# Performance work log

Measured on AMD Instinct MI355X. Metric: run time of the kernel, lower is better.

Reference implementation:

```python
import jax, jax.numpy as jnp
import numpy as np
from jax import lax

B, N = 16, 4096
S1, S2, K = 512, 256, 32
EPS = 1e-5


def setup_inputs() -> dict:
    key = jax.random.key(0)
    ks = jax.random.split(key, 8)
    p = lambda k, shape: jax.random.normal(k, shape, jnp.float32) * 0.05
    return {
        "x": jax.random.normal(ks[0], (B, 3, N), jnp.float32),
        "w1": p(ks[1], (64, 3)),
        "w2": p(ks[2], (64, 64)),
        "g1": jnp.ones(64, jnp.float32), "b1": jnp.zeros(64, jnp.float32),
        "g2": jnp.ones(64, jnp.float32), "b2": jnp.zeros(64, jnp.float32),
        "sg1_w1": p(ks[3], (128, 128)), "sg1_w2": p(ks[4], (128, 128)),
        "sg1_g1": jnp.ones(128, jnp.float32), "sg1_b1": jnp.zeros(128, jnp.float32),
        "sg1_g2": jnp.ones(128, jnp.float32), "sg1_b2": jnp.zeros(128, jnp.float32),
        "sg2_w1": p(ks[5], (256, 256)), "sg2_w2": p(ks[6], (256, 256)),
        "sg2_g1": jnp.ones(256, jnp.float32), "sg2_b1": jnp.zeros(256, jnp.float32),
        "sg2_g2": jnp.ones(256, jnp.float32), "sg2_b2": jnp.zeros(256, jnp.float32),
    }


def fps(coords, s):
    # furthest point sampling, starts at index 0 (as pointnet2 CUDA kernel)
    Bc, Nc, _ = coords.shape
    def step(carry, _):
        dist, far = carry
        centroid = jnp.take_along_axis(coords, far[:, None, None], axis=1)  # [B,1,3]
        d = jnp.sum((coords - centroid) ** 2, -1)                            # [B,N]
        dist = jnp.minimum(dist, d)
        return (dist, jnp.argmax(dist, -1)), far
    init = (jnp.full((Bc, Nc), 1e10, coords.dtype), jnp.zeros((Bc,), jnp.int32))
    _, idxs = lax.scan(step, init, None, length=s)
    return idxs.T  # [B,s]


def gather(pts, idx):
    # pts [B,N,C], idx [B,...] -> [B,...,C]
    return jax.vmap(lambda p, i: p[i])(pts, idx)


def sqdist(a, b):
    # [B,S,3],[B,N,3] -> [B,S,N]
    return (jnp.sum(a ** 2, -1)[..., None] + jnp.sum(b ** 2, -1)[:, None, :]
            - 2.0 * jnp.einsum('bsc,bnc->bsn', a, b))


def bn_relu_grouped(y, g, b):
    # y [B,s,k,O]; BatchNorm1d over (B*s, O, k) => stats over (0,1,2)
    m = y.mean((0, 1, 2), keepdims=True)
    v = y.var((0, 1, 2), keepdims=True)
    return jax.nn.relu((y - m) / jnp.sqrt(v + EPS) * g + b)


def sg_block(f_bnc, coords, s, w1, g1, b1, w2, g2, b2):
    # f_bnc [B,N,C]; coords [B,N,3]
    fidx = fps(coords, s)                      # [B,s]
    new_xyz = gather(coords, fidx)             # [B,s,3]
    new_feat = gather(f_bnc, fidx)             # [B,s,C]
    d = sqdist(new_xyz, coords)                # [B,s,N]
    _, knn_idx = lax.top_k(-d, K)              # [B,s,K]
    grouped = gather(f_bnc, knn_idx)           # [B,s,K,C]
    center = new_feat[:, :, None]              # [B,s,1,C]
    agg = jnp.concatenate([grouped - center,
                           jnp.broadcast_to(center, grouped.shape)], -1)  # [B,s,K,2C]
    y = bn_relu_grouped(jnp.einsum('bskd,od->bsko', agg, w1), g1, b1)
    y = bn_relu_grouped(jnp.einsum('bskd,od->bsko', y, w2), g2, b2)
    return new_xyz, y.max(2)                   # [B,s,O]


def point_cbr(f, w, g, b):
    # f [B,C,N]; conv1d k=1 + BN (stats over (0,2)) + relu
    y = jnp.einsum('bcn,oc->bon', f, w)
    m = y.mean((0, 2), keepdims=True)
    v = y.var((0, 2), keepdims=True)
    return jax.nn.relu((y - m) / jnp.sqrt(v + EPS) * g[None, :, None] + b[None, :, None])


def reference(x, w1, w2, g1, b1, g2, b2,
              sg1_w1, sg1_w2, sg1_g1, sg1_b1, sg1_g2, sg1_b2,
              sg2_w1, sg2_w2, sg2_g1, sg2_b1, sg2_g2, sg2_b2):
    xyz = x.transpose(0, 2, 1)                                  # [B,N,3]
    f = point_cbr(point_cbr(x, w1, g1, b1), w2, g2, b2)         # [B,64,N]
    xyz1, f1 = sg_block(f.transpose(0, 2, 1), xyz, S1,
                        sg1_w1, sg1_g1, sg1_b1, sg1_w2, sg1_g2, sg1_b2)  # f1 [B,S1,128]
    _, f2 = sg_block(f1, xyz1, S2,
                     sg2_w1, sg2_g1, sg2_b1, sg2_w2, sg2_g2, sg2_b2)     # [B,S2,256]
    return f2.transpose(0, 2, 1)                                # [B,256,S2]
```

## Files before the change

kernel.cpp:

```cpp
#include <hip/hip_runtime.h>

#define EPSF 1e-5f
#define NBINS 64
#define STATS_REGION 32768

using short8  = __attribute__((ext_vector_type(8))) short;
using float4v = __attribute__((ext_vector_type(4))) float;

__device__ __forceinline__ unsigned short f2bf(float f){
    unsigned u = __float_as_uint(f);
    unsigned r = u + 0x7FFFu + ((u >> 16) & 1u);
    return (unsigned short)(r >> 16);
}
__device__ __forceinline__ float bf2f(unsigned short h){
    return __uint_as_float(((unsigned)h) << 16);
}
__device__ __forceinline__ unsigned monou(float f){
    unsigned u = __float_as_uint(f);
    return u ^ (((unsigned)((int)u >> 31)) | 0x80000000u);
}

template<int CTRL, int RMASK>
__device__ __forceinline__ float fmax_dpp(float x){
    int xi = __float_as_int(x);
    int yi = __builtin_amdgcn_update_dpp(xi, xi, CTRL, RMASK, 0xf, false);
    return fmaxf(x, __int_as_float(yi));
}
__device__ __forceinline__ float wave_max_dpp(float x){
    x = fmax_dpp<0x111, 0xf>(x);
    x = fmax_dpp<0x112, 0xf>(x);
    x = fmax_dpp<0x114, 0xf>(x);
    x = fmax_dpp<0x118, 0xf>(x);
    x = fmax_dpp<0x142, 0xa>(x);
    x = fmax_dpp<0x143, 0xc>(x);
    return __int_as_float(__builtin_amdgcn_readlane(__float_as_int(x), 63));
}

__device__ __forceinline__ void compute_ss(const float* __restrict__ st,
                                           const float* __restrict__ g,
                                           const float* __restrict__ bb,
                                           float* lss, int C, float invCnt,
                                           int t, int TPB){
    for (int c = t; c < C; c += TPB){
        float s = 0.f, q = 0.f;
        for (int bin = 0; bin < NBINS; bin++){
            s += st[bin * 2 * C + c];
            q += st[bin * 2 * C + C + c];
        }
        float m = s * invCnt;
        float v = q * invCnt - m * m;
        float sc = g[c] / sqrtf(v + EPSF);
        lss[c] = sc;
        lss[C + c] = bb[c] - m * sc;
    }
}


__global__ __launch_bounds__(1024) void stats_x_kernel(const float* __restrict__ x,
                                                       float* __restrict__ xmom){
    int t = threadIdx.x;
    float a[9] = {0,0,0,0,0,0,0,0,0};
    for (int gid = t; gid < 65536; gid += 1024){
        int b = gid >> 12, n = gid & 4095;
        const float* xb = x + (size_t)b * 12288;
        float x0 = xb[n], x1 = xb[4096 + n], x2 = xb[8192 + n];
        a[0] += x0; a[1] += x1; a[2] += x2;
        a[3] += x0*x0; a[4] += x0*x1; a[5] += x0*x2;
        a[6] += x1*x1; a[7] += x1*x2; a[8] += x2*x2;
    }
    __shared__ float red[16][9];
    #pragma unroll
    for (int k = 0; k < 9; k++){
        float v = a[k];
        for (int o = 32; o > 0; o >>= 1) v += __shfl_down(v, o, 64);
        a[k] = v;
    }
    if ((t & 63) == 0){
        #pragma unroll
        for (int k = 0; k < 9; k++) red[t >> 6][k] = a[k];
    }
    __syncthreads();
    if (t == 0){
        #pragma unroll
        for (int k = 0; k < 9; k++){
            float s = 0.f;
            for (int w = 0; w < 16; w++) s += red[w][k];
            xmom[k] = s;
        }
    }
}

__global__ __launch_bounds__(256) void pc_fused_kernel(const float* __restrict__ x,
                                                       const float* __restrict__ w1,
                                                       const float* __restrict__ w2,
                                                       const float* __restrict__ g1,
                                                       const float* __restrict__ b1,
                                                       const float* __restrict__ xmom,
                                                       float* __restrict__ y2t){
    __shared__ float w1s[192];
    __shared__ float wt[4096];
    __shared__ float lss1[128];
    __shared__ float hS[64 * 65];
    int t = threadIdx.x;
    if (t < 192) w1s[t] = w1[t];
    for (int i = t; i < 4096; i += 256){ int o = i & 63, c = i >> 6; wt[c*64+o] = w2[o*64+c]; }
    __syncthreads();
    if (t < 64){
        float mu0 = xmom[0] * (1.f/65536.f), mu1 = xmom[1] * (1.f/65536.f), mu2 = xmom[2] * (1.f/65536.f);
        float M00 = xmom[3] * (1.f/65536.f), M01 = xmom[4] * (1.f/65536.f), M02 = xmom[5] * (1.f/65536.f);
        float M11 = xmom[6] * (1.f/65536.f), M12 = xmom[7] * (1.f/65536.f), M22 = xmom[8] * (1.f/65536.f);
        float a = w1s[t*3], b = w1s[t*3+1], c = w1s[t*3+2];
        float mo = a*mu0 + b*mu1 + c*mu2;
        float e2 = a*a*M00 + b*b*M11 + c*c*M22 + 2.f*(a*b*M01 + a*c*M02 + b*c*M12);
        float var = e2 - mo*mo;
        float sc = g1[t] / sqrtf(var + EPSF);
        lss1[t] = sc;
        lss1[64 + t] = b1[t] - mo * sc;
    }
    __syncthreads();
    int p = t & 63, cg = t >> 6;
    int point = blockIdx.x * 64 + p;
    int b = point >> 12, n = point & 4095;
    const float* xb = x + (size_t)b * 12288;
    float x0 = xb[n], x1 = xb[4096 + n], x2 = xb[8192 + n];
    #pragma unroll
    for (int i = 0; i < 16; i++){
        int c = cg * 16 + i;
        float y1 = x0 * w1s[c*3] + x1 * w1s[c*3+1] + x2 * w1s[c*3+2];
        hS[p * 65 + c] = fmaxf(y1 * lss1[c] + lss1[64 + c], 0.f);
    }
    __syncthreads();
    float4v acc[4];
    #pragma unroll
    for (int i = 0; i < 4; i++) acc[i] = (float4v){0.f,0.f,0.f,0.f};
    for (int c = 0; c < 64; c++){
        float hv = hS[p * 65 + c];
        #pragma unroll
        for (int i = 0; i < 4; i++){
            float4v w4 = *(const float4v*)&wt[c*64 + cg*16 + i*4];
            acc[i] += hv * w4;
        }
    }
    float* dst = y2t + (size_t)point * 64 + cg * 16;
    #pragma unroll
    for (int i = 0; i < 4; i++) *(float4v*)(dst + i*4) = acc[i];
}

__global__ __launch_bounds__(256) void stats_y2_kernel(const float* __restrict__ y2t,
                                                       float* __restrict__ sums){
    int t = threadIdx.x, blk = blockIdx.x;
    int o = t & 63, rg = t >> 6;
    float s = 0.f, q = 0.f;
    for (int j = 0; j < 64; j++){
        int row = blk * 256 + j * 4 + rg;
        float v = y2t[(size_t)row * 64 + o];
        s += v; q += v * v;
    }
    __shared__ float rs[4][64], rq[4][64];
    rs[rg][o] = s; rq[rg][o] = q;
    __syncthreads();
    if (t < 64){
        float ss = rs[0][t] + rs[1][t] + rs[2][t] + rs[3][t];
        float qq = rq[0][t] + rq[1][t] + rq[2][t] + rq[3][t];
        float* dst = sums + (size_t)(blk & (NBINS - 1)) * 128;
        atomicAdd(&dst[t], ss);
        atomicAdd(&dst[64 + t], qq);
    }
}

template<int NP, int SO, int TPB, bool STRIDED>
__global__ __launch_bounds__(TPB) void fps_kernel(const float* __restrict__ coords,
                                                  int* __restrict__ fidx,
                                                  float* __restrict__ xyz_out){
    __shared__ float lx[NP], ly[NP], lz[NP];
    constexpr int W = TPB / 64;
    __shared__ unsigned long long red[2][W];
    const int b = blockIdx.x, t = threadIdx.x;
    constexpr int P = NP / TPB;
    const float* cb = coords + (size_t)b * 3 * NP;
    float px[P], py[P], pz[P], dist[P];
    #pragma unroll
    for (int i = 0; i < P; i++){
        int n = i * TPB + t;
        float X, Y, Z;
        if (STRIDED){ X = cb[n]; Y = cb[NP + n]; Z = cb[2*NP + n]; }
        else        { X = cb[n*3]; Y = cb[n*3+1]; Z = cb[n*3+2]; }
        lx[n] = X; ly[n] = Y; lz[n] = Z;
    }
    __syncthreads();
    #pragma unroll
    for (int i = 0; i < P; i++){
        int n = t * P + i;
        px[i] = lx[n]; py[i] = ly[n]; pz[i] = lz[n];
        dist[i] = 1e10f;
    }
    int cur = 0;
    for (int it = 0; it < SO; ++it){
        if (t == 0){
            fidx[b * SO + it] = cur;
            float* xo = xyz_out + ((size_t)b * SO + it) * 3;
            xo[0] = lx[cur]; xo[1] = ly[cur]; xo[2] = lz[cur];
        }
        float cx = lx[cur], cy = ly[cur], cz = lz[cur];
        float bd = -1.f;
        int bn = 0;
        {
            #pragma clang fp contract(off)
            #pragma unroll
            for (int i = 0; i < P; i++){
                float dx = px[i] - cx, dy = py[i] - cy, dz = pz[i] - cz;
                float d = (dx*dx + dy*dy) + dz*dz;
                float nd = fminf(dist[i], d);
                dist[i] = nd;
                if (nd > bd){ bd = nd; bn = t * P + i; }
            }
        }
        float wm = wave_max_dpp(bd);
        unsigned long long msk = __ballot(bd == wm);
        int wl = (int)(__ffsll(msk) - 1);
        int n_w = __builtin_amdgcn_readlane(bn, wl);
        if constexpr (W == 1){
            cur = n_w;
        } else {
            int par = it & 1;
            if ((t & 63) == 0){
                red[par][t >> 6] = ((unsigned long long)__float_as_uint(wm) << 32)
                                 | (unsigned)(0xFFFFFFFFu - (unsigned)n_w);
            }
            __syncthreads();
            unsigned long long best = red[par][0];
            #pragma unroll
            for (int j = 1; j < W; j++){
                unsigned long long v = red[par][j];
                best = best > v ? best : v;
            }
            cur = (int)(0xFFFFFFFFu - (unsigned)(best & 0xFFFFFFFFull));
        }
    }
}


template<int NC, int SO, bool STRIDED>
__global__ __launch_bounds__(64) void knn_kernel(const float* __restrict__ coords,
                                                 const float* __restrict__ samp,
                                                 int* __restrict__ knno){
    const int blk = blockIdx.x;
    const int b = blk / SO, s = blk % SO;
    const int lane = threadIdx.x;
    const float* cb = coords + (size_t)b * 3 * NC;
    const float* a = samp + ((size_t)b * SO + s) * 3;
    float ax = a[0], ay = a[1], az = a[2];
    float asq = ax*ax + ay*ay + az*az;
    constexpr int J = NC / 64;
    unsigned long long t8[8];
    #pragma unroll
    for (int i = 0; i < 8; i++) t8[i] = ~0ULL;
    for (int j = 0; j < J; j++){
        int n = j * 64 + lane;
        float bx, by, bz;
        if (STRIDED){ bx = cb[n]; by = cb[NC + n]; bz = cb[2*NC + n]; }
        else        { bx = cb[n*3]; by = cb[n*3+1]; bz = cb[n*3+2]; }
        float bsq = bx*bx + by*by + bz*bz;
        float dot = ax*bx + ay*by + az*bz;
        float d = (asq + bsq) - 2.0f * dot;
        unsigned long long key = ((unsigned long long)monou(d) << 32) | (unsigned)n;
        if (key < t8[7]){
            t8[7] = key;
            #pragma unroll
            for (int i = 6; i >= 0; i--){
                if (t8[i] > t8[i+1]){ unsigned long long tm = t8[i]; t8[i] = t8[i+1]; t8[i+1] = tm; }
            }
        }
    }
    unsigned long long cur = t8[0];
    int myout = 0;
    bool bad = false;
    int popped = 0;
    for (int r = 0; r < 32; r++){
        unsigned long long m = cur;
        #pragma unroll
        for (int o2 = 32; o2 > 0; o2 >>= 1){
            unsigned long long v = __shfl_xor(m, o2, 64);
            m = m < v ? m : v;
        }
        if (lane == r) myout = (int)(unsigned)(m & 0xFFFFFFFFull);
        if (cur == m){
            #pragma unroll
            for (int i = 0; i < 7; i++) t8[i] = t8[i+1];
            t8[7] = ~0ULL;
            cur = t8[0];
            popped++;
            if (J > 8 && popped == 8 && r < 31) bad = true;
        }
    }
    if (__any(bad)){
        unsigned long long last = 0;
        for (int r = 0; r < 32; r++){
            unsigned long long mk = ~0ULL;
            for (int j = 0; j < J; j++){
                int n = j * 64 + lane;
                float bx, by, bz;
                if (STRIDED){ bx = cb[n]; by = cb[NC + n]; bz = cb[2*NC + n]; }
                else        { bx = cb[n*3]; by = cb[n*3+1]; bz = cb[n*3+2]; }
                float bsq = bx*bx + by*by + bz*bz;
                float dot = ax*bx + ay*by + az*bz;
                float d = (asq + bsq) - 2.0f * dot;
                unsigned long long key = ((unsigned long long)monou(d) << 32) | (unsigned)n;
                if (key > last && key < mk) mk = key;
            }
            unsigned long long m = mk;
            #pragma unroll
            for (int o2 = 32; o2 > 0; o2 >>= 1){
                unsigned long long v = __shfl_xor(m, o2, 64);
                m = m < v ? m : v;
            }
            if (lane == r) myout = (int)(unsigned)(m & 0xFFFFFFFFull);
            last = m;
        }
    }
    if (lane < 32) knno[((size_t)b * SO + s) * 32 + lane] = myout;
}


template<int O, int D>
__device__ __forceinline__ void pack_body(const float* __restrict__ w,
                                          unsigned short* __restrict__ pk, int tid){
    constexpr int CH = D / 32;
    constexpr int TOT = (O/16) * CH * 64;
    if (tid >= TOT) return;
    int lane = tid & 63;
    int fc = tid >> 6;
    int ch = fc % CH;
    int ot = fc / CH;
    int o  = ot * 16 + (lane & 15);
    int kb = ch * 32 + (lane >> 4) * 8;
    #pragma unroll
    for (int j = 0; j < 8; j++) pk[(size_t)tid * 8 + j] = f2bf(w[(size_t)o * D + kb + j]);
}

__global__ __launch_bounds__(256) void pack_all_kernel(const float* w1, const float* w2,
                                                       const float* w3, const float* w4,
                                                       unsigned short* p1, unsigned short* p2,
                                                       unsigned short* p3, unsigned short* p4){
    int blk = blockIdx.x, t = threadIdx.x;
    if (blk < 8)       pack_body<128,128>(w1, p1, blk * 256 + t);
    else if (blk < 16) pack_body<128,128>(w2, p2, (blk - 8) * 256 + t);
    else if (blk < 48) pack_body<256,256>(w3, p3, (blk - 16) * 256 + t);
    else               pack_body<256,256>(w4, p4, (blk - 48) * 256 + t);
}

template<int D, int O>
__device__ __forceinline__ void mfma_store_y(const short* A, const short* wp,
                                             unsigned short* Y, float* lsum, float* lsq,
                                             int blk, int t){
    constexpr int RS = D + 8;
    constexpr int CH = D / 32;
    constexpr int OT = O / 16;
    constexpr int OPW = OT / 4;
    int lane = t & 63, wv = t >> 6;
    int col = lane & 15, quad = lane >> 4;
    for (int oi = 0; oi < OPW; ++oi){
        int ot = wv * OPW + oi;
        for (int mt = 0; mt < 4; ++mt){
            float4v acc = {0.f, 0.f, 0.f, 0.f};
            #pragma unroll
            for (int ch = 0; ch < CH; ++ch){
                short8 a  = *(const short8*)(A + (mt*16 + col) * RS + ch*32 + quad*8);
                short8 bf = *(const short8*)(wp + ((size_t)(ot*CH + ch) * 64 + lane) * 8);
                acc = __builtin_amdgcn_mfma_f32_16x16x32_bf16(a, bf, acc, 0, 0, 0);
            }
            float s4 = 0.f, q4 = 0.f;
            size_t rowbase = (size_t)blk * 64 + mt * 16 + quad * 4;
            #pragma unroll
            for (int r = 0; r < 4; r++){
                float v = acc[r];
                s4 += v; q4 += v * v;
                Y[(rowbase + r) * O + ot * 16 + col] = f2bf(v);
            }
            s4 += __shfl_xor(s4, 16, 64); s4 += __shfl_xor(s4, 32, 64);
            q4 += __shfl_xor(q4, 16, 64); q4 += __shfl_xor(q4, 32, 64);
            if (quad == 0){ lsum[ot*16 + col] += s4; lsq[ot*16 + col] += q4; }
        }
    }
}

template<int D, int O>
__device__ __forceinline__ void mfma_maxmin(const short* A, const short* wp,
                                            float2* mxmn, float* lsum, float* lsq,
                                            int blk, int t){
    constexpr int RS = D + 8;
    constexpr int CH = D / 32;
    constexpr int OT = O / 16;
    constexpr int OPW = OT / 4;
    int lane = t & 63, wv = t >> 6;
    int col = lane & 15, quad = lane >> 4;
    for (int oi = 0; oi < OPW; ++oi){
        int ot = wv * OPW + oi;
        float mx[2] = {-1e30f, -1e30f}, mn[2] = {1e30f, 1e30f};
        for (int mt = 0; mt < 4; ++mt){
            float4v acc = {0.f, 0.f, 0.f, 0.f};
            #pragma unroll
            for (int ch = 0; ch < CH; ++ch){
                short8 a  = *(const short8*)(A + (mt*16 + col) * RS + ch*32 + quad*8);
                short8 bf = *(const short8*)(wp + ((size_t)(ot*CH + ch) * 64 + lane) * 8);
                acc = __builtin_amdgcn_mfma_f32_16x16x32_bf16(a, bf, acc, 0, 0, 0);
            }
            int g = mt >> 1;
            float s4 = 0.f, q4 = 0.f;
            #pragma unroll
            for (int r = 0; r < 4; r++){
                float v = acc[r];
                s4 += v; q4 += v * v;
                mx[g] = fmaxf(mx[g], v);
                mn[g] = fminf(mn[g], v);
            }
            s4 += __shfl_xor(s4, 16, 64); s4 += __shfl_xor(s4, 32, 64);
            q4 += __shfl_xor(q4, 16, 64); q4 += __shfl_xor(q4, 32, 64);
            if (quad == 0){ lsum[ot*16 + col] += s4; lsq[ot*16 + col] += q4; }
        }
        #pragma unroll
        for (int g = 0; g < 2; g++){
            mx[g] = fmaxf(mx[g], __shfl_xor(mx[g], 16, 64));
            mx[g] = fmaxf(mx[g], __shfl_xor(mx[g], 32, 64));
            mn[g] = fminf(mn[g], __shfl_xor(mn[g], 16, 64));
            mn[g] = fminf(mn[g], __shfl_xor(mn[g], 32, 64));
            if (quad == 0){
                mxmn[((size_t)(blk * 2 + g)) * O + ot * 16 + col] = make_float2(mx[g], mn[g]);
            }
        }
    }
}

template<int DH, int O, int S, int NPTS, int MODE>
__global__ __launch_bounds__(256) void gemm1_kernel(const void* __restrict__ fsrc,
                                                    const float* __restrict__ fst,
                                                    const float* __restrict__ fg,
                                                    const float* __restrict__ fb,
                                                    float finv,
                                                    const int* __restrict__ fidx,
                                                    const int* __restrict__ knn,
                                                    const short* __restrict__ wp,
                                                    unsigned short* __restrict__ Y,
                                                    float* __restrict__ sums){
    constexpr int D = 2 * DH;
    constexpr int RS = D + 8;
    __shared__ __align__(16) short A[64 * RS];
    __shared__ float lsum[O], lsq[O];
    __shared__ float lssf[2 * DH];
    int t = threadIdx.x;
    for (int i = t; i < O; i += 256){ lsum[i] = 0.f; lsq[i] = 0.f; }
    compute_ss(fst, fg, fb, lssf, DH, finv, t, 256);
    __syncthreads();
    int blk = blockIdx.x;
    for (int g = 0; g < 2; ++g){
        int gid = blk * 2 + g;
        int b = gid / S;
        int cidx = fidx[gid];
        int kk = t >> 3;
        int p  = t & 7;
        int nb = knn[(size_t)gid * 32 + kk];
        constexpr int E = D / 8;
        int d0 = p * E;
        short* row = A + (g * 32 + kk) * RS;
        if (MODE == 1){
            const float* fcp = (const float*)fsrc + ((size_t)b * NPTS + cidx) * DH;
            const float* fnp = (const float*)fsrc + ((size_t)b * NPTS + nb) * DH;
            #pragma unroll
            for (int e = 0; e < E; e++){
                int d = d0 + e;
                float v;
                if (d < DH){
                    float a = fmaxf(fnp[d] * lssf[d] + lssf[DH + d], 0.f);
                    float c = fmaxf(fcp[d] * lssf[d] + lssf[DH + d], 0.f);
                    v = a - c;
                } else {
                    v = fmaxf(fcp[d - DH] * lssf[d - DH] + lssf[DH + d - DH], 0.f);
                }
                row[d] = (short)f2bf(v);
            }
        } else {
            const float2* fcp = (const float2*)fsrc + ((size_t)b * NPTS + cidx) * DH;
            const float2* fnp = (const float2*)fsrc + ((size_t)b * NPTS + nb) * DH;
            #pragma unroll
            for (int e = 0; e < E; e++){
                int d = d0 + e;
                float v;
                if (d < DH){
                    float sc = lssf[d], sh = lssf[DH + d];
                    float2 a2 = fnp[d], c2 = fcp[d];
                    float av = fmaxf((sc > 0.f ? a2.x : a2.y) * sc + sh, 0.f);
                    float cv = fmaxf((sc > 0.f ? c2.x : c2.y) * sc + sh, 0.f);
                    v = av - cv;
                } else {
                    int dd = d - DH;
                    float sc = lssf[dd], sh = lssf[DH + dd];
                    float2 c2 = fcp[dd];
                    v = fmaxf((sc > 0.f ? c2.x : c2.y) * sc + sh, 0.f);
                }
                row[d] = (short)f2bf(v);
            }
        }
    }
    __syncthreads();
    mfma_store_y<D, O>(A, wp, Y, lsum, lsq, blk, t);
    __syncthreads();
    float* dst = sums + (size_t)(blk & (NBINS - 1)) * 2 * O;
    for (int i = t; i < O; i += 256){
        atomicAdd(&dst[i], lsum[i]);
        atomicAdd(&dst[O + i], lsq[i]);
    }
}

template<int D, int O>
__global__ __launch_bounds__(256) void gemm2m_kernel(const unsigned short* __restrict__ Yin,
                                                     const float* __restrict__ st,
                                                     const float* __restrict__ g,
                                                     const float* __restrict__ bb,
                                                     float inv,
                                                     const short* __restrict__ wp,
                                                     float2* __restrict__ mxmn,
                                                     float* __restrict__ sums){
    constexpr int RS = D + 8;
    __shared__ __align__(16) short A[64 * RS];
    __shared__ float lsum[O], lsq[O];
    __shared__ float lss[2 * D];
    int t = threadIdx.x;
    for (int i = t; i < O; i += 256){ lsum[i] = 0.f; lsq[i] = 0.f; }
    compute_ss(st, g, bb, lss, D, inv, t, 256);
    __syncthreads();
    int blk = blockIdx.x;
    {
        int row = t >> 2;
        int d0 = (t & 3) * (D / 4);
        const unsigned short* src = Yin + ((size_t)blk * 64 + row) * D + d0;
        short* dst = A + row * RS + d0;
        #pragma unroll
        for (int e = 0; e < D/4; e++){
            float v = bf2f(src[e]);
            int d = d0 + e;
            v = fmaxf(v * lss[d] + lss[D + d], 0.f);
            dst[e] = (short)f2bf(v);
        }
    }
    __syncthreads();
    mfma_maxmin<D, O>(A, wp, mxmn, lsum, lsq, blk, t);
    __syncthreads();
    float* dst = sums + (size_t)(blk & (NBINS - 1)) * 2 * O;
    for (int i = t; i < O; i += 256){
        atomicAdd(&dst[i], lsum[i]);
        atomicAdd(&dst[O + i], lsq[i]);
    }
}

__global__ __launch_bounds__(256) void final_out_kernel(const float2* __restrict__ mxmn,
                                                        const float* __restrict__ st,
                                                        const float* __restrict__ g,
                                                        const float* __restrict__ bb,
                                                        float inv,
                                                        float* __restrict__ out){
    __shared__ float lss[512];
    __shared__ float tile[64][65];
    int t = threadIdx.x;
    compute_ss(st, g, bb, lss, 256, inv, t, 256);
    __syncthreads();
    int blk = blockIdx.x;
    int b = blk >> 4;
    int ot = (blk >> 2) & 3, stt = blk & 3;
    int o_in = t & 63, sg = t >> 6;
    int o = ot * 64 + o_in;
    float sc = lss[o], sh = lss[256 + o];
    for (int si = 0; si < 16; si++){
        int s = stt * 64 + sg * 16 + si;
        int row = b * 256 + s;
        float2 v2 = mxmn[(size_t)row * 256 + o];
        float v = (sc > 0.f ? v2.x : v2.y) * sc + sh;
        tile[sg * 16 + si][o_in] = fmaxf(v, 0.f);
    }
    __syncthreads();
    int s_in = t & 63, og = t >> 6;
    for (int oj = 0; oj < 16; oj++){
        int oo = ot * 64 + og * 16 + oj;
        out[(size_t)b * 65536 + (size_t)oo * 256 + stt * 64 + s_in] = tile[s_in][og * 16 + oj];
    }
}

extern "C" void kernel_launch(void* const* d_in, const int* in_sizes, int n_in,
                              void* d_out, int out_size, void* d_ws, size_t ws_size,
                              hipStream_t stream) {
    const float* x    = (const float*)d_in[0];
    const float* w1   = (const float*)d_in[1];
    const float* w2   = (const float*)d_in[2];
    const float* g1   = (const float*)d_in[3];
    const float* b1   = (const float*)d_in[4];
    const float* g2   = (const float*)d_in[5];
    const float* b2   = (const float*)d_in[6];
    const float* s1w1 = (const float*)d_in[7];
    const float* s1w2 = (const float*)d_in[8];
    const float* s1g1 = (const float*)d_in[9];
    const float* s1b1 = (const float*)d_in[10];
    const float* s1g2 = (const float*)d_in[11];
    const float* s1b2 = (const float*)d_in[12];
    const float* s2w1 = (const float*)d_in[13];
    const float* s2w2 = (const float*)d_in[14];
    const float* s2g1 = (const float*)d_in[15];
    const float* s2b1 = (const float*)d_in[16];
    const float* s2g2 = (const float*)d_in[17];
    const float* s2b2 = (const float*)d_in[18];
    float* out = (float*)d_out;

    char* ws = (char*)d_ws;
    size_t off = 0;
    auto take = [&](size_t bytes){ size_t r = off; off += (bytes + 255) & ~(size_t)255; return r; };
    float* y2t     = (float*)(ws + take(16u*4096u*64u*4u));
    float2* mxmn1  = (float2*)(ws + take(8192u*128u*8u));
    float2* mxmn2  = (float2*)(ws + take(4096u*256u*8u));
    int*   fidx1   = (int*)  (ws + take(16u*512u*4u));
    float* xyz1    = (float*)(ws + take(16u*512u*3u*4u));
    int*   fidx2   = (int*)  (ws + take(16u*256u*4u));
    float* xyz2    = (float*)(ws + take(16u*256u*3u*4u));
    int*   knn1    = (int*)  (ws + take(16u*512u*32u*4u));
    int*   knn2    = (int*)  (ws + take(16u*256u*32u*4u));
    unsigned short* wp1 = (unsigned short*)(ws + take(128u*128u*2u));
    unsigned short* wp2 = (unsigned short*)(ws + take(128u*128u*2u));
    unsigned short* wp3 = (unsigned short*)(ws + take(256u*256u*2u));
    unsigned short* wp4 = (unsigned short*)(ws + take(256u*256u*2u));
    float* stats   = (float*)(ws + take(6u*STATS_REGION*4u));
    char*  regA    = ws + take(67108864u);
    (void)in_sizes; (void)n_in; (void)out_size; (void)ws_size;

    float* xmom    = stats + 0*STATS_REGION;
    float* stY2    = stats + 1*STATS_REGION;
    float* stG1a   = stats + 2*STATS_REGION;
    float* stG2a   = stats + 3*STATS_REGION;
    float* stG1b   = stats + 4*STATS_REGION;
    float* stG2b   = stats + 5*STATS_REGION;

    hipMemsetAsync(stats, 0, 6u*STATS_REGION*4u, stream);

    pack_all_kernel<<<80, 256, 0, stream>>>(s1w1, s1w2, s2w1, s2w2, wp1, wp2, wp3, wp4);

    stats_x_kernel<<<1, 1024, 0, stream>>>(x, xmom);
    pc_fused_kernel<<<1024, 256, 0, stream>>>(x, w1, w2, g1, b1, xmom, y2t);
    stats_y2_kernel<<<256, 256, 0, stream>>>(y2t, stY2);

    fps_kernel<4096,512,256,true><<<16, 256, 0, stream>>>(x, fidx1, xyz1);
    knn_kernel<4096,512,true><<<8192, 64, 0, stream>>>(x, xyz1, knn1);

    unsigned short* Y1 = (unsigned short*)regA;
    gemm1_kernel<64,128,512,4096,1><<<4096, 256, 0, stream>>>(
        y2t, stY2, g2, b2, 1.f/65536.f, fidx1, knn1, (const short*)wp1, Y1, stG1a);
    gemm2m_kernel<128,128><<<4096, 256, 0, stream>>>(
        Y1, stG1a, s1g1, s1b1, 1.f/262144.f, (const short*)wp2, mxmn1, stG2a);

    fps_kernel<512,256,64,false><<<16, 64, 0, stream>>>(xyz1, fidx2, xyz2);
    knn_kernel<512,256,false><<<4096, 64, 0, stream>>>(xyz1, xyz2, knn2);

    gemm1_kernel<128,256,256,512,2><<<2048, 256, 0, stream>>>(
        mxmn1, stG2a, s1g2, s1b2, 1.f/262144.f, fidx2, knn2, (const short*)wp3, Y1, stG1b);
    gemm2m_kernel<256,256><<<2048, 256, 0, stream>>>(
        Y1, stG1b, s2g1, s2b1, 1.f/131072.f, (const short*)wp4, mxmn2, stG2b);
    final_out_kernel<<<256, 256, 0, stream>>>(
        mxmn2, stG2b, s2g2, s2b2, 1.f/131072.f, out);
}
```

Measured before the change: 1.029 ms.

## Merge independent stages into combined kernels to overlap FPS with GEMM work

Independent pipeline stages are packed into shared launches by splitting on block index. Examples are FPS1 with the pointwise conv, stats_y2 with knn1, FPS2 with the first grouped GEMM, and knn2 with the second GEMM. Kernel bodies become device functions using dynamic shared memory. The intent is to hide the long serial FPS loops under parallel work and cut launch count. A risk is that heterogeneous blocks share resource limits (shared memory sized for the larger body), which may reduce occupancy of the GEMM parts.

```diff
diff --git a/kernel.cpp b/kernel.cpp
--- a/kernel.cpp
+++ b/kernel.cpp
@@ -55,139 +55,29 @@
     }
 }
 
-
-__global__ __launch_bounds__(1024) void stats_x_kernel(const float* __restrict__ x,
-                                                       float* __restrict__ xmom){
-    int t = threadIdx.x;
-    float a[9] = {0,0,0,0,0,0,0,0,0};
-    for (int gid = t; gid < 65536; gid += 1024){
-        int b = gid >> 12, n = gid & 4095;
-        const float* xb = x + (size_t)b * 12288;
-        float x0 = xb[n], x1 = xb[4096 + n], x2 = xb[8192 + n];
-        a[0] += x0; a[1] += x1; a[2] += x2;
-        a[3] += x0*x0; a[4] += x0*x1; a[5] += x0*x2;
-        a[6] += x1*x1; a[7] += x1*x2; a[8] += x2*x2;
-    }
-    __shared__ float red[16][9];
+template<int NP, int SO, int AW, bool STRIDED>
+__device__ void fps_body(char* smem, const float* __restrict__ coords,
+                         int* __restrict__ fidx, float* __restrict__ xyz_out, int b){
+    float* lx = (float*)smem;
+    float* ly = lx + NP;
+    float* lz = ly + NP;
+    unsigned long long* red = (unsigned long long*)(lz + NP);
+    const int t = threadIdx.x;
+    const float* cb = coords + (size_t)b * 3 * NP;
+    constexpr int PS = NP / 256;
     #pragma unroll
-    for (int k = 0; k < 9; k++){
-        float v = a[k];
-        for (int o = 32; o > 0; o >>= 1) v += __shfl_down(v, o, 64);
-        a[k] = v;
-    }
-    if ((t & 63) == 0){
-        #pragma unroll
-        for (int k = 0; k < 9; k++) red[t >> 6][k] = a[k];
-    }
-    __syncthreads();
-    if (t == 0){
-        #pragma unroll
-        for (int k = 0; k < 9; k++){
-            float s = 0.f;
-            for (int w = 0; w < 16; w++) s += red[w][k];
-            xmom[k] = s;
-        }
-    }
-}
-
-__global__ __launch_bounds__(256) void pc_fused_kernel(const float* __restrict__ x,
-                                                       const float* __restrict__ w1,
-                                                       const float* __restrict__ w2,
-                                                       const float* __restrict__ g1,
-                                                       const float* __restrict__ b1,
-                                                       const float* __restrict__ xmom,
-                                                       float* __restrict__ y2t){
-    __shared__ float w1s[192];
-    __shared__ float wt[4096];
-    __shared__ float lss1[128];
-    __shared__ float hS[64 * 65];
-    int t = threadIdx.x;
-    if (t < 192) w1s[t] = w1[t];
-    for (int i = t; i < 4096; i += 256){ int o = i & 63, c = i >> 6; wt[c*64+o] = w2[o*64+c]; }
-    __syncthreads();
-    if (t < 64){
-        float mu0 = xmom[0] * (1.f/65536.f), mu1 = xmom[1] * (1.f/65536.f), mu2 = xmom[2] * (1.f/65536.f);
-        float M00 = xmom[3] * (1.f/65536.f), M01 = xmom[4] * (1.f/65536.f), M02 = xmom[5] * (1.f/65536.f);
-        float M11 = xmom[6] * (1.f/65536.f), M12 = xmom[7] * (1.f/65536.f), M22 = xmom[8] * (1.f/65536.f);
-        float a = w1s[t*3], b = w1s[t*3+1], c = w1s[t*3+2];
-        float mo = a*mu0 + b*mu1 + c*mu2;
-        float e2 = a*a*M00 + b*b*M11 + c*c*M22 + 2.f*(a*b*M01 + a*c*M02 + b*c*M12);
-        float var = e2 - mo*mo;
-        float sc = g1[t] / sqrtf(var + EPSF);
-        lss1[t] = sc;
-        lss1[64 + t] = b1[t] - mo * sc;
-    }
-    __syncthreads();
-    int p = t & 63, cg = t >> 6;
-    int point = blockIdx.x * 64 + p;
-    int b = point >> 12, n = point & 4095;
-    const float* xb = x + (size_t)b * 12288;
-    float x0 = xb[n], x1 = xb[4096 + n], x2 = xb[8192 + n];
-    #pragma unroll
-    for (int i = 0; i < 16; i++){
-        int c = cg * 16 + i;
-        float y1 = x0 * w1s[c*3] + x1 * w1s[c*3+1] + x2 * w1s[c*3+2];
-        hS[p * 65 + c] = fmaxf(y1 * lss1[c] + lss1[64 + c], 0.f);
-    }
-    __syncthreads();
-    float4v acc[4];
-    #pragma unroll
-    for (int i = 0; i < 4; i++) acc[i] = (float4v){0.f,0.f,0.f,0.f};
-    for (int c = 0; c < 64; c++){
-        float hv = hS[p * 65 + c];
-        #pragma unroll
-        for (int i = 0; i < 4; i++){
-            float4v w4 = *(const float4v*)&wt[c*64 + cg*16 + i*4];
-            acc[i] += hv * w4;
-        }
-    }
-    float* dst = y2t + (size_t)point * 64 + cg * 16;
-    #pragma unroll
-    for (int i = 0; i < 4; i++) *(float4v*)(dst + i*4) = acc[i];
-}
-
-__global__ __launch_bounds__(256) void stats_y2_kernel(const float* __restrict__ y2t,
-                                                       float* __restrict__ sums){
-    int t = threadIdx.x, blk = blockIdx.x;
-    int o = t & 63, rg = t >> 6;
-    float s = 0.f, q = 0.f;
-    for (int j = 0; j < 64; j++){
-        int row = blk * 256 + j * 4 + rg;
-        float v = y2t[(size_t)row * 64 + o];
-        s += v; q += v * v;
-    }
-    __shared__ float rs[4][64], rq[4][64];
-    rs[rg][o] = s; rq[rg][o] = q;
-    __syncthreads();
-    if (t < 64){
-        float ss = rs[0][t] + rs[1][t] + rs[2][t] + rs[3][t];
-        float qq = rq[0][t] + rq[1][t] + rq[2][t] + rq[3][t];
-        float* dst = sums + (size_t)(blk & (NBINS - 1)) * 128;
-        atomicAdd(&dst[t], ss);
-        atomicAdd(&dst[64 + t], qq);
-    }
-}
-
-template<int NP, int SO, int TPB, bool STRIDED>
-__global__ __launch_bounds__(TPB) void fps_kernel(const float* __restrict__ coords,
-                                                  int* __restrict__ fidx,
-                                                  float* __restrict__ xyz_out){
-    __shared__ float lx[NP], ly[NP], lz[NP];
-    constexpr int W = TPB / 64;
-    __shared__ unsigned long long red[2][W];
-    const int b = blockIdx.x, t = threadIdx.x;
-    constexpr int P = NP / TPB;
-    const float* cb = coords + (size_t)b * 3 * NP;
-    float px[P], py[P], pz[P], dist[P];
-    #pragma unroll
-    for (int i = 0; i < P; i++){
-        int n = i * TPB + t;
+    for (int i = 0; i < PS; i++){
+        int n = i * 256 + t;
         float X, Y, Z;
         if (STRIDED){ X = cb[n]; Y = cb[NP + n]; Z = cb[2*NP + n]; }
         else        { X = cb[n*3]; Y = cb[n*3+1]; Z = cb[n*3+2]; }
         lx[n] = X; ly[n] = Y; lz[n] = Z;
     }
     __syncthreads();
+    if (AW == 1 && t >= 64) return;
+    constexpr int TPB = AW * 64;
+    constexpr int P = NP / TPB;
+    float px[P], py[P], pz[P], dist[P];
     #pragma unroll
     for (int i = 0; i < P; i++){
         int n = t * P + i;
@@ -219,19 +109,19 @@
         unsigned long long msk = __ballot(bd == wm);
         int wl = (int)(__ffsll(msk) - 1);
         int n_w = __builtin_amdgcn_readlane(bn, wl);
-        if constexpr (W == 1){
+        if constexpr (AW == 1){
             cur = n_w;
         } else {
             int par = it & 1;
             if ((t & 63) == 0){
-                red[par][t >> 6] = ((unsigned long long)__float_as_uint(wm) << 32)
-                                 | (unsigned)(0xFFFFFFFFu - (unsigned)n_w);
+                red[par * AW + (t >> 6)] = ((unsigned long long)__float_as_uint(wm) << 32)
+                                         | (unsigned)(0xFFFFFFFFu - (unsigned)n_w);
             }
             __syncthreads();
-            unsigned long long best = red[par][0];
-            #pragma unroll
-            for (int j = 1; j < W; j++){
-                unsigned long long v = red[par][j];
+            unsigned long long best = red[par * AW];
+            #pragma unroll
+            for (int j = 1; j < AW; j++){
+                unsigned long long v = red[par * AW + j];
                 best = best > v ? best : v;
             }
             cur = (int)(0xFFFFFFFFu - (unsigned)(best & 0xFFFFFFFFull));
@@ -239,14 +129,12 @@
     }
 }
 
-
 template<int NC, int SO, bool STRIDED>
-__global__ __launch_bounds__(64) void knn_kernel(const float* __restrict__ coords,
-                                                 const float* __restrict__ samp,
-                                                 int* __restrict__ knno){
-    const int blk = blockIdx.x;
-    const int b = blk / SO, s = blk % SO;
-    const int lane = threadIdx.x;
+__device__ void knn_body(const float* __restrict__ coords,
+                         const float* __restrict__ samp,
+                         int* __restrict__ knno, int row){
+    const int b = row / SO, s = row % SO;
+    const int lane = threadIdx.x & 63;
     const float* cb = coords + (size_t)b * 3 * NC;
     const float* a = samp + ((size_t)b * SO + s) * 3;
     float ax = a[0], ay = a[1], az = a[2];
@@ -321,6 +209,59 @@
     if (lane < 32) knno[((size_t)b * SO + s) * 32 + lane] = myout;
 }
 
+__device__ void pc_body(char* smem, const float* __restrict__ x,
+                        const float* __restrict__ w1, const float* __restrict__ w2,
+                        const float* __restrict__ g1, const float* __restrict__ b1,
+                        const float* __restrict__ xmom, float* __restrict__ y2t, int blk){
+    float* w1s  = (float*)smem;
+    float* wt   = w1s + 192;
+    float* lss1 = wt + 4096;
+    float* hS   = lss1 + 128;
+    int t = threadIdx.x;
+    if (t < 192) w1s[t] = w1[t];
+    for (int i = t; i < 4096; i += 256){ int o = i & 63, c = i >> 6; wt[c*64+o] = w2[o*64+c]; }
+    __syncthreads();
+    if (t < 64){
+        float mu0 = xmom[0] * (1.f/65536.f), mu1 = xmom[1] * (1.f/65536.f), mu2 = xmom[2] * (1.f/65536.f);
+        float M00 = xmom[3] * (1.f/65536.f), M01 = xmom[4] * (1.f/65536.f), M02 = xmom[5] * (1.f/65536.f);
+        float M11 = xmom[6] * (1.f/65536.f), M12 = xmom[7] * (1.f/65536.f), M22 = xmom[8] * (1.f/65536.f);
+        float a = w1s[t*3], b = w1s[t*3+1], c = w1s[t*3+2];
+        float mo = a*mu0 + b*mu1 + c*mu2;
+        float e2 = a*a*M00 + b*b*M11 + c*c*M22 + 2.f*(a*b*M01 + a*c*M02 + b*c*M12);
+        float var = e2 - mo*mo;
+        float sc = g1[t] / sqrtf(var + EPSF);
+        lss1[t] = sc;
+        lss1[64 + t] = b1[t] - mo * sc;
+    }
+    __syncthreads();
+    int p = t & 63, cg = t >> 6;
+    int point = blk * 64 + p;
+    int b = point >> 12, n = point & 4095;
+    const float* xb = x + (size_t)b * 12288;
+    float x0 = xb[n], x1 = xb[4096 + n], x2 = xb[8192 + n];
+    #pragma unroll
+    for (int i = 0; i < 16; i++){
+        int c = cg * 16 + i;
+        float y1 = x0 * w1s[c*3] + x1 * w1s[c*3+1] + x2 * w1s[c*3+2];
+        hS[p * 65 + c] = fmaxf(y1 * lss1[c] + lss1[64 + c], 0.f);
+    }
+    __syncthreads();
+    float4v acc[4];
+    #pragma unroll
+    for (int i = 0; i < 4; i++) acc[i] = (float4v){0.f,0.f,0.f,0.f};
+    for (int c = 0; c < 64; c++){
+        float hv = hS[p * 65 + c];
+        #pragma unroll
+        for (int i = 0; i < 4; i++){
+            float4v w4 = *(const float4v*)&wt[c*64 + cg*16 + i*4];
+            acc[i] += hv * w4;
+        }
+    }
+    float* dst = y2t + (size_t)point * 64 + cg * 16;
+    #pragma unroll
+    for (int i = 0; i < 4; i++) *(float4v*)(dst + i*4) = acc[i];
+}
+
 
 template<int O, int D>
 __device__ __forceinline__ void pack_body(const float* __restrict__ w,
@@ -338,25 +279,13 @@
     for (int j = 0; j < 8; j++) pk[(size_t)tid * 8 + j] = f2bf(w[(size_t)o * D + kb + j]);
 }
 
-__global__ __launch_bounds__(256) void pack_all_kernel(const float* w1, const float* w2,
-                                                       const float* w3, const float* w4,
-                                                       unsigned short* p1, unsigned short* p2,
-                                                       unsigned short* p3, unsigned short* p4){
-    int blk = blockIdx.x, t = threadIdx.x;
-    if (blk < 8)       pack_body<128,128>(w1, p1, blk * 256 + t);
-    else if (blk < 16) pack_body<128,128>(w2, p2, (blk - 8) * 256 + t);
-    else if (blk < 48) pack_body<256,256>(w3, p3, (blk - 16) * 256 + t);
-    else               pack_body<256,256>(w4, p4, (blk - 48) * 256 + t);
-}
-
 template<int D, int O>
 __device__ __forceinline__ void mfma_store_y(const short* A, const short* wp,
                                              unsigned short* Y, float* lsum, float* lsq,
                                              int blk, int t){
     constexpr int RS = D + 8;
     constexpr int CH = D / 32;
-    constexpr int OT = O / 16;
-    constexpr int OPW = OT / 4;
+    constexpr int OPW = (O / 16) / 4;
     int lane = t & 63, wv = t >> 6;
     int col = lane & 15, quad = lane >> 4;
     for (int oi = 0; oi < OPW; ++oi){
@@ -390,8 +319,7 @@
                                             int blk, int t){
     constexpr int RS = D + 8;
     constexpr int CH = D / 32;
-    constexpr int OT = O / 16;
-    constexpr int OPW = OT / 4;
+    constexpr int OPW = (O / 16) / 4;
     int lane = t & 63, wv = t >> 6;
     int col = lane & 15, quad = lane >> 4;
     for (int oi = 0; oi < OPW; ++oi){
@@ -432,26 +360,22 @@
 }
 
 template<int DH, int O, int S, int NPTS, int MODE>
-__global__ __launch_bounds__(256) void gemm1_kernel(const void* __restrict__ fsrc,
-                                                    const float* __restrict__ fst,
-                                                    const float* __restrict__ fg,
-                                                    const float* __restrict__ fb,
-                                                    float finv,
-                                                    const int* __restrict__ fidx,
-                                                    const int* __restrict__ knn,
-                                                    const short* __restrict__ wp,
-                                                    unsigned short* __restrict__ Y,
-                                                    float* __restrict__ sums){
+__device__ void gemm1_body(char* smem, const void* __restrict__ fsrc,
+                           const float* __restrict__ fst, const float* __restrict__ fg,
+                           const float* __restrict__ fb, float finv,
+                           const int* __restrict__ fidx, const int* __restrict__ knn,
+                           const short* __restrict__ wp, unsigned short* __restrict__ Y,
+                           float* __restrict__ sums, int blk){
     constexpr int D = 2 * DH;
     constexpr int RS = D + 8;
-    __shared__ __align__(16) short A[64 * RS];
-    __shared__ float lsum[O], lsq[O];
-    __shared__ float lssf[2 * DH];
+    short* A    = (short*)smem;
+    float* lsum = (float*)(smem + 64*RS*2);
+    float* lsq  = lsum + O;
+    float* lssf = lsq + O;
     int t = threadIdx.x;
     for (int i = t; i < O; i += 256){ lsum[i] = 0.f; lsq[i] = 0.f; }
     compute_ss(fst, fg, fb, lssf, DH, finv, t, 256);
     __syncthreads();
-    int blk = blockIdx.x;
     for (int g = 0; g < 2; ++g){
         int gid = blk * 2 + g;
         int b = gid / S;
@@ -512,23 +436,20 @@
 }
 
 template<int D, int O>
-__global__ __launch_bounds__(256) void gemm2m_kernel(const unsigned short* __restrict__ Yin,
-                                                     const float* __restrict__ st,
-                                                     const float* __restrict__ g,
-                                                     const float* __restrict__ bb,
-                                                     float inv,
-                                                     const short* __restrict__ wp,
-                                                     float2* __restrict__ mxmn,
-                                                     float* __restrict__ sums){
+__device__ void gemm2m_body(char* smem, const unsigned short* __restrict__ Yin,
+                            const float* __restrict__ st, const float* __restrict__ g,
+                            const float* __restrict__ bb, float inv,
+                            const short* __restrict__ wp, float2* __restrict__ mxmn,
+                            float* __restrict__ sums, int blk){
     constexpr int RS = D + 8;
-    __shared__ __align__(16) short A[64 * RS];
-    __shared__ float lsum[O], lsq[O];
-    __shared__ float lss[2 * D];
+    short* A    = (short*)smem;
+    float* lsum = (float*)(smem + 64*RS*2);
+    float* lsq  = lsum + O;
+    float* lss  = lsq + O;
     int t = threadIdx.x;
     for (int i = t; i < O; i += 256){ lsum[i] = 0.f; lsq[i] = 0.f; }
     compute_ss(st, g, bb, lss, D, inv, t, 256);
     __syncthreads();
-    int blk = blockIdx.x;
     {
         int row = t >> 2;
         int d0 = (t & 3) * (D / 4);
@@ -550,6 +471,147 @@
         atomicAdd(&dst[i], lsum[i]);
         atomicAdd(&dst[O + i], lsq[i]);
     }
+}
+
+
+__global__ __launch_bounds__(256) void k1_statsx_pack(const float* __restrict__ x,
+                                                      float* __restrict__ xmom,
+                                                      const float* w1, const float* w2,
+                                                      const float* w3, const float* w4,
+                                                      unsigned short* p1, unsigned short* p2,
+                                                      unsigned short* p3, unsigned short* p4){
+    int blk = blockIdx.x, t = threadIdx.x;
+    if (blk == 0){
+        float a[9] = {0,0,0,0,0,0,0,0,0};
+        for (int gid = t; gid < 65536; gid += 256){
+            int b = gid >> 12, n = gid & 4095;
+            const float* xb = x + (size_t)b * 12288;
+            float x0 = xb[n], x1 = xb[4096 + n], x2 = xb[8192 + n];
+            a[0] += x0; a[1] += x1; a[2] += x2;
+            a[3] += x0*x0; a[4] += x0*x1; a[5] += x0*x2;
+            a[6] += x1*x1; a[7] += x1*x2; a[8] += x2*x2;
+        }
+        __shared__ float red[4][9];
+        #pragma unroll
+        for (int k = 0; k < 9; k++){
+            float v = a[k];
+            for (int o = 32; o > 0; o >>= 1) v += __shfl_down(v, o, 64);
+            a[k] = v;
+        }
+        if ((t & 63) == 0){
+            #pragma unroll
+            for (int k = 0; k < 9; k++) red[t >> 6][k] = a[k];
+        }
+        __syncthreads();
+        if (t == 0){
+            #pragma unroll
+            for (int k = 0; k < 9; k++)
+                xmom[k] = red[0][k] + red[1][k] + red[2][k] + red[3][k];
+        }
+    } else {
+        int pb = blk - 1;
+        if (pb < 8)       pack_body<128,128>(w1, p1, pb * 256 + t);
+        else if (pb < 16) pack_body<128,128>(w2, p2, (pb - 8) * 256 + t);
+        else if (pb < 48) pack_body<256,256>(w3, p3, (pb - 16) * 256 + t);
+        else              pack_body<256,256>(w4, p4, (pb - 48) * 256 + t);
+    }
+}
+
+__global__ __launch_bounds__(256) void k2_fps1_pc(const float* __restrict__ x,
+                                                  int* __restrict__ fidx1, float* __restrict__ xyz1,
+                                                  const float* w1, const float* w2,
+                                                  const float* g1, const float* b1,
+                                                  const float* __restrict__ xmom,
+                                                  float* __restrict__ y2t){
+    extern __shared__ char smem[];
+    if (blockIdx.x < 16) fps_body<4096,512,4,true>(smem, x, fidx1, xyz1, blockIdx.x);
+    else                 pc_body(smem, x, w1, w2, g1, b1, xmom, y2t, blockIdx.x - 16);
+}
+
+__global__ __launch_bounds__(256) void k3_statsy2_knn1(const float* __restrict__ y2t,
+                                                       float* __restrict__ stY2,
+                                                       const float* __restrict__ x,
+                                                       const float* __restrict__ xyz1,
+                                                       int* __restrict__ knn1){
+    int t = threadIdx.x;
+    if (blockIdx.x < 256){
+        int blk = blockIdx.x;
+        int o = t & 63, rg = t >> 6;
+        float s = 0.f, q = 0.f;
+        for (int j = 0; j < 64; j++){
+            int row = blk * 256 + j * 4 + rg;
+            float v = y2t[(size_t)row * 64 + o];
+            s += v; q += v * v;
+        }
+        __shared__ float rs[4][64], rq[4][64];
+        rs[rg][o] = s; rq[rg][o] = q;
+        __syncthreads();
+        if (t < 64){
+            float ss = rs[0][t] + rs[1][t] + rs[2][t] + rs[3][t];
+            float qq = rq[0][t] + rq[1][t] + rq[2][t] + rq[3][t];
+            float* dst = stY2 + (size_t)(blk & (NBINS - 1)) * 128;
+            atomicAdd(&dst[t], ss);
+            atomicAdd(&dst[64 + t], qq);
+        }
+    } else {
+        int row = (blockIdx.x - 256) * 4 + (t >> 6);
+        knn_body<4096,512,true>(x, xyz1, knn1, row);
+    }
+}
+
+__global__ __launch_bounds__(256) void k4_fps2_gemm1a(const float* __restrict__ xyz1,
+                                                      int* __restrict__ fidx2, float* __restrict__ xyz2,
+                                                      const float* __restrict__ y2t,
+                                                      const float* __restrict__ stY2,
+                                                      const float* g2, const float* b2,
+                                                      const int* __restrict__ fidx1,
+                                                      const int* __restrict__ knn1,
+                                                      const short* __restrict__ wp1,
+                                                      unsigned short* __restrict__ Y1,
+                                                      float* __restrict__ stG1a){
+    extern __shared__ char smem[];
+    if (blockIdx.x < 16)
+        fps_body<512,256,1,false>(smem, xyz1, fidx2, xyz2, blockIdx.x);
+    else
+        gemm1_body<64,128,512,4096,1>(smem, y2t, stY2, g2, b2, 1.f/65536.f,
+                                      fidx1, knn1, wp1, Y1, stG1a, blockIdx.x - 16);
+}
+
+__global__ __launch_bounds__(256) void k5_knn2_gemm2ma(const float* __restrict__ xyz1,
+                                                       const float* __restrict__ xyz2,
+                                                       int* __restrict__ knn2,
+                                                       const unsigned short* __restrict__ Y1,
+                                                       const float* __restrict__ stG1a,
+                                                       const float* s1g1, const float* s1b1,
+                                                       const short* __restrict__ wp2,
+                                                       float2* __restrict__ mxmn1,
+                                                       float* __restrict__ stG2a){
+    extern __shared__ char smem[];
+    if (blockIdx.x < 1024){
+        int row = blockIdx.x * 4 + (threadIdx.x >> 6);
+        knn_body<512,256,false>(xyz1, xyz2, knn2, row);
+    } else {
+        gemm2m_body<128,128>(smem, Y1, stG1a, s1g1, s1b1, 1.f/262144.f,
+                             wp2, mxmn1, stG2a, blockIdx.x - 1024);
+    }
+}
+
+template<int DH, int O, int S, int NPTS, int MODE>
+__global__ __launch_bounds__(256) void gemm1_kernel(const void* fsrc, const float* fst,
+                                                    const float* fg, const float* fb, float finv,
+                                                    const int* fidx, const int* knn,
+                                                    const short* wp, unsigned short* Y,
+                                                    float* sums){
+    extern __shared__ char smem[];
+    gemm1_body<DH,O,S,NPTS,MODE>(smem, fsrc, fst, fg, fb, finv, fidx, knn, wp, Y, sums, blockIdx.x);
+}
+
+template<int D, int O>
+__global__ __launch_bounds__(256) void gemm2m_kernel(const unsigned short* Yin, const float* st,
+                                                     const float* g, const float* bb, float inv,
+                                                     const short* wp, float2* mxmn, float* sums){
+    extern __shared__ char smem[];
+    gemm2m_body<D,O>(smem, Yin, st, g, bb, inv, wp, mxmn, sums, blockIdx.x);
 }
 
 __global__ __launch_bounds__(256) void final_out_kernel(const float2* __restrict__ mxmn,
@@ -635,30 +697,20 @@
     float* stG1b   = stats + 4*STATS_REGION;
     float* stG2b   = stats + 5*STATS_REGION;
 
+    unsigned short* Y1 = (unsigned short*)regA;
+
     hipMemsetAsync(stats, 0, 6u*STATS_REGION*4u, stream);
 
-    pack_all_kernel<<<80, 256, 0, stream>>>(s1w1, s1w2, s2w1, s2w2, wp1, wp2, wp3, wp4);
-
-    stats_x_kernel<<<1, 1024, 0, stream>>>(x, xmom);
-    pc_fused_kernel<<<1024, 256, 0, stream>>>(x, w1, w2, g1, b1, xmom, y2t);
-    stats_y2_kernel<<<256, 256, 0, stream>>>(y2t, stY2);
-
-    fps_kernel<4096,512,256,true><<<16, 256, 0, stream>>>(x, fidx1, xyz1);
-    knn_kernel<4096,512,true><<<8192, 64, 0, stream>>>(x, xyz1, knn1);
-
-    unsigned short* Y1 = (unsigned short*)regA;
-    gemm1_kernel<64,128,512,4096,1><<<4096, 256, 0, stream>>>(
-        y2t, stY2, g2, b2, 1.f/65536.f, fidx1, knn1, (const short*)wp1, Y1, stG1a);
-    gemm2m_kernel<128,128><<<4096, 256, 0, stream>>>(
-        Y1, stG1a, s1g1, s1b1, 1.f/262144.f, (const short*)wp2, mxmn1, stG2a);
-
-    fps_kernel<512,256,64,false><<<16, 64, 0, stream>>>(xyz1, fidx2, xyz2);
-    knn_kernel<512,256,false><<<4096, 64, 0, stream>>>(xyz1, xyz2, knn2);
-
-    gemm1_kernel<128,256,256,512,2><<<2048, 256, 0, stream>>>(
+    k1_statsx_pack<<<81, 256, 0, stream>>>(x, xmom, s1w1, s1w2, s2w1, s2w2, wp1, wp2, wp3, wp4);
+    k2_fps1_pc<<<1040, 256, 49216, stream>>>(x, fidx1, xyz1, w1, w2, g1, b1, xmom, y2t);
+    k3_statsy2_knn1<<<2304, 256, 0, stream>>>(y2t, stY2, x, xyz1, knn1);
+    k4_fps2_gemm1a<<<4112, 256, 18944, stream>>>(xyz1, fidx2, xyz2, y2t, stY2, g2, b2,
+                                                 fidx1, knn1, (const short*)wp1, Y1, stG1a);
+    k5_knn2_gemm2ma<<<5120, 256, 19456, stream>>>(xyz1, xyz2, knn2, Y1, stG1a, s1g1, s1b1,
+                                                  (const short*)wp2, mxmn1, stG2a);
+    gemm1_kernel<128,256,256,512,2><<<2048, 256, 36864, stream>>>(
         mxmn1, stG2a, s1g2, s1b2, 1.f/262144.f, fidx2, knn2, (const short*)wp3, Y1, stG1b);
-    gemm2m_kernel<256,256><<<2048, 256, 0, stream>>>(
+    gemm2m_kernel<256,256><<<2048, 256, 37888, stream>>>(
         Y1, stG1b, s2g1, s2b1, 1.f/131072.f, (const short*)wp4, mxmn2, stG2b);
-    final_out_kernel<<<256, 256, 0, stream>>>(
-        mxmn2, stG2b, s2g2, s2b2, 1.f/131072.f, out);
-}
+    final_out_kernel<<<256, 256, 0, stream>>>(mxmn2, stG2b, s2g2, s2b2, 1.f/131072.f, out);
+}
```

Measured after the change: 979.1 us. 1.05x faster.
